# Performance work log

Hardware: AMD Instinct MI355X
Metric: run time of the kernel (lower is better)

Reference implementation:

```python
import jax, jax.numpy as jnp
import numpy as np

A = 15        # action_size
N = 3         # n_rollouts
TEMP = 1.0    # temperature
GAMMA = 0.99
D = 256       # state / embedder input dim
H = 256       # mid_weight == embedder output_dim
B = 32


def _mlp3(x, W0, b0, W1, b1, W2, b2):
    h = jax.nn.relu(x @ W0 + b0)
    h = jax.nn.relu(h @ W1 + b1)
    return h @ W2 + b2


def setup_inputs() -> dict:
    key = jax.random.key(0)
    ks = iter(jax.random.split(key, 32))

    def lin(i, o):
        return jax.random.normal(next(ks), (i, o), jnp.float32) * (1.0 / np.sqrt(i))

    inp = {"x": jax.random.normal(next(ks), (B, D), jnp.float32)}
    # embedder MLP: D -> H -> H -> H
    inp.update(emb_W0=lin(D, H), emb_b0=jnp.zeros((H,), jnp.float32),
               emb_W1=lin(H, H), emb_b1=jnp.zeros((H,), jnp.float32),
               emb_W2=lin(H, H), emb_b2=jnp.zeros((H,), jnp.float32))
    # fc_value: H -> 1
    inp.update(v_W=lin(H, 1), v_b=jnp.zeros((1,), jnp.float32))
    # cont_rew MLP: D+1 -> H -> H -> 2 (done logit, reward)
    inp.update(cr_W0=lin(D + 1, H), cr_b0=jnp.zeros((H,), jnp.float32),
               cr_W1=lin(H, H), cr_b1=jnp.zeros((H,), jnp.float32),
               cr_W2=lin(H, 2), cr_b2=jnp.zeros((2,), jnp.float32))
    # transition model MLP: D+1 -> H -> H -> D
    inp.update(tm_W0=lin(D + 1, H), tm_b0=jnp.zeros((H,), jnp.float32),
               tm_W1=lin(H, H), tm_b1=jnp.zeros((H,), jnp.float32),
               tm_W2=lin(H, D), tm_b2=jnp.zeros((D,), jnp.float32))
    return inp


def reference(x, emb_W0, emb_b0, emb_W1, emb_b1, emb_W2, emb_b2,
              v_W, v_b,
              cr_W0, cr_b0, cr_W1, cr_b1, cr_W2, cr_b2,
              tm_W0, tm_b0, tm_W1, tm_b1, tm_W2, tm_b2):
    def value(s):  # [..., D] -> [...]
        e = _mlp3(s, emb_W0, emb_b0, emb_W1, emb_b1, emb_W2, emb_b2)
        return (e @ v_W + v_b)[..., 0]

    acts = jnp.arange(A, dtype=x.dtype)

    v = value(x)  # [B]

    s = x
    rews, cont = [], []
    for _ in range(N):
        # states_with_all_actions: [..., A, D+1]
        sA = jnp.broadcast_to(s[..., None, :], s.shape[:-1] + (A, s.shape[-1]))
        aA = jnp.broadcast_to(acts, s.shape[:-1] + (A,))
        sa = jnp.concatenate([sA, aA[..., None]], axis=-1)
        dr = _mlp3(sa, cr_W0, cr_b0, cr_W1, cr_b1, cr_W2, cr_b2)  # [..., A, 2]
        cont.append(jax.nn.sigmoid(dr[..., 0]))
        rews.append(dr[..., 1])
        # transition for all actions at once; new action axis goes to dim 1
        ns = _mlp3(sa, tm_W0, tm_b0, tm_W1, tm_b1, tm_W2, tm_b2)  # [..., A, D]
        s = jnp.moveaxis(ns, -2, 1)

    cum = jnp.zeros_like(rews[0])  # [B, A]
    for r in rews[:-1]:
        c = (cum + r) * GAMMA
        cum = jnp.broadcast_to(c[..., None, :], c.shape[:-1] + (A,) + c.shape[-1:])

    vs = value(s) * (GAMMA ** N) + cum  # [B] + [A]*N
    for i in range(N - 1):
        vs = jnp.where(jnp.round(cont[-(i + 1)]) == 1, 0.0, vs)
        w = jax.nn.softmax(vs / TEMP, axis=-1)
        vs = (w * vs).sum(-1)

    log_probs = jax.nn.log_softmax(vs / TEMP, axis=1)  # [B, A]
    return log_probs, v
```

## Files before the change

kernel.cpp:

```cpp
#include <hip/hip_runtime.h>

#define NA 15
#define NB 32
#define DD 256
#define PL 65536
#define ASTR 264

using bf16x8 = __attribute__((ext_vector_type(8))) short;
using f32x4  = __attribute__((ext_vector_type(4))) float;

__device__ __forceinline__ unsigned short f2bf(float f){
  unsigned int u = __float_as_uint(f);
  u = u + 0x7fffu + ((u >> 16) & 1u);
  return (unsigned short)(u >> 16);
}
__device__ __forceinline__ float bf2f(unsigned short h){
  return __uint_as_float(((unsigned int)h) << 16);
}
__device__ __forceinline__ unsigned int cvtpk_bf16(float lo, float hi){
    unsigned int r;
    asm("v_cvt_pk_bf16_f32 %0, %1, %2" : "=v"(r) : "v"(lo), "v"(hi));
    return r;
}
__device__ __forceinline__ void split1_write(const float v[4], short* pH){
    unsigned int h01 = cvtpk_bf16(v[0], v[1]);
    unsigned int h23 = cvtpk_bf16(v[2], v[3]);
    *(uint2*)pH = make_uint2(h01, h23);
}
__device__ __forceinline__ void split2_write(const float v[4], short* pH, short* pL){
    unsigned int h01 = cvtpk_bf16(v[0], v[1]);
    unsigned int h23 = cvtpk_bf16(v[2], v[3]);
    float r0 = v[0] - __uint_as_float(h01 << 16);
    float r1 = v[1] - __uint_as_float(h01 & 0xffff0000u);
    float r2 = v[2] - __uint_as_float(h23 << 16);
    float r3 = v[3] - __uint_as_float(h23 & 0xffff0000u);
    unsigned int l01 = cvtpk_bf16(r0, r1);
    unsigned int l23 = cvtpk_bf16(r2, r3);
    *(uint2*)pH = make_uint2(h01, h23);
    *(uint2*)pL = make_uint2(l01, l23);
}
__device__ __forceinline__ void split3_write(const float v[4], short* pH, short* pM, short* pL){
    unsigned int h01 = cvtpk_bf16(v[0], v[1]);
    unsigned int h23 = cvtpk_bf16(v[2], v[3]);
    float r0 = v[0] - __uint_as_float(h01 << 16);
    float r1 = v[1] - __uint_as_float(h01 & 0xffff0000u);
    float r2 = v[2] - __uint_as_float(h23 << 16);
    float r3 = v[3] - __uint_as_float(h23 & 0xffff0000u);
    unsigned int m01 = cvtpk_bf16(r0, r1);
    unsigned int m23 = cvtpk_bf16(r2, r3);
    float s0 = r0 - __uint_as_float(m01 << 16);
    float s1 = r1 - __uint_as_float(m01 & 0xffff0000u);
    float s2 = r2 - __uint_as_float(m23 << 16);
    float s3 = r3 - __uint_as_float(m23 & 0xffff0000u);
    unsigned int l01 = cvtpk_bf16(s0, s1);
    unsigned int l23 = cvtpk_bf16(s2, s3);
    *(uint2*)pH = make_uint2(h01, h23);
    *(uint2*)pM = make_uint2(m01, m23);
    *(uint2*)pL = make_uint2(l01, l23);
}

template<int TM, bool RELU>
__device__ __forceinline__ void layer256(
    const float* __restrict__ W, const float* __restrict__ bias,
    const float* act, int K, int lda, float* out, int ldo)
{
    constexpr int RPG = TM / 4;
    const int tid = threadIdx.x;
    const int tr = tid >> 6;
    const int tc = tid & 63;
    float acc[RPG][4];
#pragma unroll
    for (int i = 0; i < RPG; ++i) { acc[i][0]=0.f; acc[i][1]=0.f; acc[i][2]=0.f; acc[i][3]=0.f; }
    const float* wp = W + 4 * tc;
    int k = 0;
    for (; k + 4 <= K; k += 4) {
        float4 w0 = *reinterpret_cast<const float4*>(wp + (k + 0) * DD);
        float4 w1 = *reinterpret_cast<const float4*>(wp + (k + 1) * DD);
        float4 w2 = *reinterpret_cast<const float4*>(wp + (k + 2) * DD);
        float4 w3 = *reinterpret_cast<const float4*>(wp + (k + 3) * DD);
#pragma unroll
        for (int i = 0; i < RPG; ++i) {
            float4 a = *reinterpret_cast<const float4*>(act + (RPG * tr + i) * lda + k);
            acc[i][0] += a.x * w0.x + a.y * w1.x + a.z * w2.x + a.w * w3.x;
            acc[i][1] += a.x * w0.y + a.y * w1.y + a.z * w2.y + a.w * w3.y;
            acc[i][2] += a.x * w0.z + a.y * w1.z + a.z * w2.z + a.w * w3.z;
            acc[i][3] += a.x * w0.w + a.y * w1.w + a.z * w2.w + a.w * w3.w;
        }
    }
    for (; k < K; ++k) {
        float4 w0 = *reinterpret_cast<const float4*>(wp + k * DD);
#pragma unroll
        for (int i = 0; i < RPG; ++i) {
            float a = act[(RPG * tr + i) * lda + k];
            acc[i][0] += a * w0.x; acc[i][1] += a * w0.y;
            acc[i][2] += a * w0.z; acc[i][3] += a * w0.w;
        }
    }
    float4 bb = *reinterpret_cast<const float4*>(bias + 4 * tc);
#pragma unroll
    for (int i = 0; i < RPG; ++i) {
        float4 o;
        o.x = acc[i][0] + bb.x; o.y = acc[i][1] + bb.y;
        o.z = acc[i][2] + bb.z; o.w = acc[i][3] + bb.w;
        if (RELU) {
            o.x = fmaxf(o.x, 0.f); o.y = fmaxf(o.y, 0.f);
            o.z = fmaxf(o.z, 0.f); o.w = fmaxf(o.w, 0.f);
        }
        *reinterpret_cast<float4*>(out + (RPG * tr + i) * ldo + 4 * tc) = o;
    }
}

template<int TM>
__device__ __forceinline__ void head1c(
    const float* h, int ldh, const float* __restrict__ W, int wstr, int col, float bias,
    float* __restrict__ gout, int gbase)
{
    const int wv = threadIdx.x >> 6;
    const int lane = threadIdx.x & 63;
    for (int rr = wv; rr < TM; rr += 4) {
        float p = 0.f;
#pragma unroll
        for (int t = 0; t < 4; ++t) {
            int k = lane + 64 * t;
            p += h[rr * ldh + k] * W[k * wstr + col];
        }
#pragma unroll
        for (int m = 1; m < 64; m <<= 1) p += __shfl_xor(p, m);
        if (lane == 0) gout[gbase + rr] = p + bias;
    }
}

__global__ __launch_bounds__(256) void front_kernel(
    const float* __restrict__ x,
    const float* __restrict__ emW0, const float* __restrict__ emB0,
    const float* __restrict__ emW1, const float* __restrict__ emB1,
    const float* __restrict__ emW2, const float* __restrict__ emB2,
    const float* __restrict__ vW, const float* __restrict__ vb,
    const float* __restrict__ crW0, const float* __restrict__ crW1,
    const float* __restrict__ tmW0, const float* __restrict__ tmW1,
    const float* __restrict__ tmW2, const float* __restrict__ tmB2,
    short* __restrict__ planes, float* __restrict__ w5, float* __restrict__ b5,
    float* __restrict__ c2cr, float* __restrict__ c2tm, float* __restrict__ b45,
    float* __restrict__ vout, float* __restrict__ U1cr, float* __restrict__ U1tm)
{
    __shared__ __align__(16) float smem[32 * DD];
    const int blk = blockIdx.x;
    const int tid = threadIdx.x;

    if (blk < 24) {
        const int mat = blk >> 3;
        const int kk  = blk & 7;
        const float* W = (mat == 0) ? crW1 : (mat == 1) ? tmW1 : emW1;
        const int col = tid;
        short bh[32], bm[32], bl[32];
#pragma unroll
        for (int j = 0; j < 32; ++j) {
            float w = W[(kk * 32 + j) * 256 + col];
            unsigned short h = f2bf(w); float fh = bf2f(h);
            float r1 = w - fh;
            unsigned short m = f2bf(r1); float fm = bf2f(m);
            bh[j] = (short)h; bm[j] = (short)m; bl[j] = (short)f2bf(r1 - fm);
        }
        short* pH = planes + (size_t)(mat * 3 + 0) * PL + kk * 8192 + col * 32;
        short* pM = planes + (size_t)(mat * 3 + 1) * PL + kk * 8192 + col * 32;
        short* pLp = planes + (size_t)(mat * 3 + 2) * PL + kk * 8192 + col * 32;
#pragma unroll
        for (int j = 0; j < 32; j += 4) {
            *(short4*)(pH + j) = make_short4(bh[j], bh[j+1], bh[j+2], bh[j+3]);
            *(short4*)(pM + j) = make_short4(bm[j], bm[j+1], bm[j+2], bm[j+3]);
            *(short4*)(pLp + j) = make_short4(bl[j], bl[j+1], bl[j+2], bl[j+3]);
        }
    } else if (blk == 24) {
        float acc = 0.f;
        for (int j = 0; j < 256; j += 4) {
            float4 wrow = *(const float4*)(emW2 + tid * 256 + j);
            float4 vv   = *(const float4*)(vW + j);
            acc += wrow.x * vv.x + wrow.y * vv.y + wrow.z * vv.z + wrow.w * vv.w;
        }
        w5[tid] = acc;
        if (tid == 0) {
            float b = 0.f;
            for (int j = 0; j < 256; ++j) b += emB2[j] * vW[j];
            b5[0] = b + vb[0];
        }
    } else if (blk < 33) {
        constexpr int TM = 4;
        float* bufA = smem;
        float* bufB = bufA + TM * DD;
        float* bufC = bufB + TM * DD;
        const int row0 = (blk - 25) * TM;
        for (int i = 0; i < TM; ++i) bufA[i * DD + tid] = x[(row0 + i) * DD + tid];
        __syncthreads();
        layer256<TM, true >(emW0, emB0, bufA, 256, DD, bufB, DD); __syncthreads();
        layer256<TM, true >(emW1, emB1, bufB, 256, DD, bufC, DD); __syncthreads();
        layer256<TM, false>(emW2, emB2, bufC, 256, DD, bufB, DD); __syncthreads();
        head1c<TM>(bufB, DD, vW, 1, 0, vb[0], vout, row0);
    } else if (blk < 41) {
        const int row0 = (blk - 33) * 4;
        float* xs = smem;
        for (int i = 0; i < 4; ++i) xs[i * 256 + tid] = x[(row0 + i) * 256 + tid];
        __syncthreads();
        float acr[4] = {0.f,0.f,0.f,0.f}, atm[4] = {0.f,0.f,0.f,0.f};
        for (int k = 0; k < 256; ++k) {
            float wc = crW0[k * 256 + tid];
            float wt = tmW0[k * 256 + tid];
#pragma unroll
            for (int i = 0; i < 4; ++i) {
                acr[i] += xs[i * 256 + k] * wc;
                atm[i] += xs[i * 256 + k] * wt;
            }
        }
        for (int i = 0; i < 4; ++i) {
            U1cr[(row0 + i) * 256 + tid] = acr[i];
            U1tm[(row0 + i) * 256 + tid] = atm[i];
        }
    } else if (blk < 65) {
        const int pb = blk - 41;
        const int prod = pb >> 3;
        const int r0 = (pb & 7) * 32;
        const float* B = (prod == 0) ? emW0 : (prod == 1) ? crW0 : tmW0;
        const int pbase = 9 + prod * 3;
        float* As = smem;
        for (int i = tid; i < 32 * 256; i += 256)
            As[i] = tmW2[(r0 + (i >> 8)) * 256 + (i & 255)];
        __syncthreads();
        float acc[32];
#pragma unroll
        for (int j = 0; j < 32; ++j) acc[j] = 0.f;
        for (int m = 0; m < 256; ++m) {
            float b = B[m * 256 + tid];
#pragma unroll
            for (int j = 0; j < 32; ++j) acc[j] += As[j * 256 + m] * b;
        }
        short bh[32], bm[32], bl[32];
#pragma unroll
        for (int j = 0; j < 32; ++j) {
            float w = acc[j];
            unsigned short h = f2bf(w); float fh = bf2f(h);
            float r1 = w - fh;
            unsigned short mm = f2bf(r1); float fm = bf2f(mm);
            bh[j] = (short)h; bm[j] = (short)mm; bl[j] = (short)f2bf(r1 - fm);
        }
        const int kk = r0 >> 5;
        short* pH = planes + (size_t)(pbase + 0) * PL + kk * 8192 + tid * 32;
        short* pM = planes + (size_t)(pbase + 1) * PL + kk * 8192 + tid * 32;
        short* pLp = planes + (size_t)(pbase + 2) * PL + kk * 8192 + tid * 32;
#pragma unroll
        for (int j = 0; j < 32; j += 4) {
            *(short4*)(pH + j) = make_short4(bh[j], bh[j+1], bh[j+2], bh[j+3]);
            *(short4*)(pM + j) = make_short4(bm[j], bm[j+1], bm[j+2], bm[j+3]);
            *(short4*)(pLp + j) = make_short4(bl[j], bl[j+1], bl[j+2], bl[j+3]);
        }
    } else {
        const int j = tid;
        float a0 = 0.f, a1 = 0.f, a2 = 0.f;
        for (int k = 0; k < 256; ++k) {
            float t = tmB2[k];
            a0 += t * crW0[k * 256 + j];
            a1 += t * tmW0[k * 256 + j];
            a2 += t * emW0[k * 256 + j];
        }
        c2cr[j] = a0;
        c2tm[j] = a1;
        b45[j] = a2 + emB0[j];
    }
}

__global__ __launch_bounds__(256) void finalize_kernel(
    const float* __restrict__ Vns3, const float* __restrict__ cont2,
    const float* __restrict__ rews0, const float* __restrict__ rews1,
    const float* __restrict__ cont1, float* __restrict__ out)
{
    const int b = blockIdx.x;
    const int tid = threadIdx.x;
    __shared__ float vs2[NA][NA];
    __shared__ float vs3[NA];
    if (tid < NA * NA) {
        const int x = tid / NA, y = tid % NA;
        float vals[NA];
        float m = -INFINITY;
#pragma unroll
        for (int z = 0; z < NA; ++z) {
            int vidx = ((b * NA + y) * NA + z) * NA + x;
            int cidx = ((b * NA + x) * NA + y) * NA + z;
            float c1 = rews0[b * NA + z] * 0.99f;
            float c2 = (c1 + rews1[(b * NA + x) * NA + z]) * 0.99f;
            float v = Vns3[vidx] * 0.970299f + c2;
            if (cont2[cidx] > 0.f) v = 0.f;
            vals[z] = v;
            m = fmaxf(m, v);
        }
        float se = 0.f, sw = 0.f;
#pragma unroll
        for (int z = 0; z < NA; ++z) { float e = expf(vals[z] - m); se += e; sw += e * vals[z]; }
        vs2[x][y] = sw / se;
    }
    __syncthreads();
    if (tid < NA) {
        const int x = tid;
        float vals[NA];
        float m = -INFINITY;
#pragma unroll
        for (int y = 0; y < NA; ++y) {
            float v = vs2[x][y];
            if (cont1[(b * NA + x) * NA + y] > 0.f) v = 0.f;
            vals[y] = v;
            m = fmaxf(m, v);
        }
        float se = 0.f, sw = 0.f;
#pragma unroll
        for (int y = 0; y < NA; ++y) { float e = expf(vals[y] - m); se += e; sw += e * vals[y]; }
        vs3[x] = sw / se;
    }
    __syncthreads();
    if (tid == 0) {
        float m = -INFINITY;
#pragma unroll
        for (int x = 0; x < NA; ++x) m = fmaxf(m, vs3[x]);
        float se = 0.f;
#pragma unroll
        for (int x = 0; x < NA; ++x) se += expf(vs3[x] - m);
        float l = logf(se);
#pragma unroll
        for (int x = 0; x < NA; ++x) out[b * NA + x] = vs3[x] - m - l;
    }
}

template<int RT, int NP>
__device__ __forceinline__ void mm3(
    const short* __restrict__ plH, const short* __restrict__ plM, const short* __restrict__ plL,
    const short* actH, const short* actM, const short* actL,
    f32x4 (&acc)[4][RT])
{
    const int tid = threadIdx.x;
    const int ln15 = tid & 15, lng = (tid >> 4) & 3, wv = tid >> 6;
    const int wo = (wv * 64 + ln15) * 32 + lng * 8;
#pragma unroll
    for (int kk = 0; kk < 8; ++kk) {
        bf16x8 wH[4], wM[4], wL[4], xH[RT], xM[RT], xL[RT];
#pragma unroll
        for (int ct = 0; ct < 4; ++ct) {
            wH[ct] = *(const bf16x8*)(plH + wo + kk * 8192 + ct * 512);
            wM[ct] = *(const bf16x8*)(plM + wo + kk * 8192 + ct * 512);
            if (NP == 6) wL[ct] = *(const bf16x8*)(plL + wo + kk * 8192 + ct * 512);
        }
#pragma unroll
        for (int rt = 0; rt < RT; ++rt) {
            int off = (rt * 16 + ln15) * ASTR + kk * 32 + lng * 8;
            xH[rt] = *(const bf16x8*)(actH + off);
            xM[rt] = *(const bf16x8*)(actM + off);
            if (NP == 6) xL[rt] = *(const bf16x8*)(actL + off);
        }
        __builtin_amdgcn_s_setprio(1);
#pragma unroll
        for (int ct = 0; ct < 4; ++ct)
#pragma unroll
            for (int rt = 0; rt < RT; ++rt) {
                acc[ct][rt] = __builtin_amdgcn_mfma_f32_16x16x32_bf16(wH[ct], xH[rt], acc[ct][rt], 0, 0, 0);
                acc[ct][rt] = __builtin_amdgcn_mfma_f32_16x16x32_bf16(wH[ct], xM[rt], acc[ct][rt], 0, 0, 0);
                acc[ct][rt] = __builtin_amdgcn_mfma_f32_16x16x32_bf16(wM[ct], xH[rt], acc[ct][rt], 0, 0, 0);
                if (NP == 6) {
                    acc[ct][rt] = __builtin_amdgcn_mfma_f32_16x16x32_bf16(wM[ct], xM[rt], acc[ct][rt], 0, 0, 0);
                    acc[ct][rt] = __builtin_amdgcn_mfma_f32_16x16x32_bf16(wH[ct], xL[rt], acc[ct][rt], 0, 0, 0);
                    acc[ct][rt] = __builtin_amdgcn_mfma_f32_16x16x32_bf16(wL[ct], xH[rt], acc[ct][rt], 0, 0, 0);
                }
            }
        __builtin_amdgcn_s_setprio(0);
    }
}

template<int ROWS, bool CLAMP>
__device__ __forceinline__ void stage3w(
    const float* __restrict__ U, const float* __restrict__ wrow256,
    const float* __restrict__ bias, int row0,
    short* actH, short* actM, short* actL)
{
    const int tid = threadIdx.x;
    const int wv = tid >> 6, ln = tid & 63;
    constexpr int RPW = ROWS / 4;
    const float4 wr = *(const float4*)(wrow256 + ln * 4);
    const float4 bb = *(const float4*)(bias + ln * 4);
    for (int i = wv * RPW; i < wv * RPW + RPW; ++i) {
        int r = row0 + i;
        int srow = r / 15;
        if (CLAMP && srow > 7199) srow = 7199;
        float a = (float)(r % 15);
        float4 u = *(const float4*)(U + srow * 256 + ln * 4);
        float sv[4];
        sv[0] = fmaxf(u.x + a * wr.x + bb.x, 0.f);
        sv[1] = fmaxf(u.y + a * wr.y + bb.y, 0.f);
        sv[2] = fmaxf(u.z + a * wr.z + bb.z, 0.f);
        sv[3] = fmaxf(u.w + a * wr.w + bb.w, 0.f);
        split3_write(sv, actH + i * ASTR + ln * 4, actM + i * ASTR + ln * 4, actL + i * ASTR + ln * 4);
    }
}

__global__ __launch_bounds__(256, 2) void stage1m_kernel(
    const float* __restrict__ U1cr, const float* __restrict__ U1tm,
    const short* __restrict__ planes,
    const float* __restrict__ crW0, const float* __restrict__ crB0,
    const float* __restrict__ crB1, const float* __restrict__ crW2, const float* __restrict__ crB2,
    const float* __restrict__ tmW0, const float* __restrict__ tmB0,
    const float* __restrict__ tmB1,
    const float* __restrict__ c2cr, const float* __restrict__ c2tm,
    float* __restrict__ rews0, float* __restrict__ U2cr, float* __restrict__ U2tm)
{
    __shared__ short actH[16 * ASTR];
    __shared__ short actM[16 * ASTR];
    __shared__ short actL[16 * ASTR];
    __shared__ float hred[64];
    const int tid = threadIdx.x;
    const int row0 = blockIdx.x * 16;
    const int ln15 = tid & 15, lng = (tid >> 4) & 3, wv = tid >> 6;

    stage3w<16, false>(U1cr, crW0 + 65536, crB0, row0, actH, actM, actL);
    __syncthreads();
    {
        f32x4 acc[4][1];
#pragma unroll
        for (int a = 0; a < 4; ++a) acc[a][0] = f32x4{0.f,0.f,0.f,0.f};
        mm3<1, 6>(planes + 0*PL, planes + 1*PL, planes + 2*PL, actH, actM, actL, acc);
        float hp = 0.f;
#pragma unroll
        for (int ct = 0; ct < 4; ++ct) {
            const int colb = wv * 64 + ct * 16 + lng * 4;
            const float4 b1 = *(const float4*)(crB1 + colb);
            f32x4 v = acc[ct][0];
            v[0] += b1.x; v[1] += b1.y; v[2] += b1.z; v[3] += b1.w;
#pragma unroll
            for (int j = 0; j < 4; ++j) v[j] = fmaxf(v[j], 0.f);
#pragma unroll
            for (int j = 0; j < 4; ++j) hp += v[j] * crW2[(colb + j) * 2 + 1];
        }
        hp += __shfl_xor(hp, 16);
        hp += __shfl_xor(hp, 32);
        if (lng == 0) hred[wv * 16 + ln15] = hp;
        __syncthreads();
        if (tid < 16) rews0[row0 + tid] = hred[tid] + hred[16 + tid] + hred[32 + tid] + hred[48 + tid] + crB2[1];
        __syncthreads();
    }

    stage3w<16, false>(U1tm, tmW0 + 65536, tmB0, row0, actH, actM, actL);
    __syncthreads();
    {
        f32x4 acc[4][1];
#pragma unroll
        for (int a = 0; a < 4; ++a) acc[a][0] = f32x4{0.f,0.f,0.f,0.f};
        mm3<1, 6>(planes + 3*PL, planes + 4*PL, planes + 5*PL, actH, actM, actL, acc);
        __syncthreads();
#pragma unroll
        for (int ct = 0; ct < 4; ++ct) {
            const int colb = wv * 64 + ct * 16 + lng * 4;
            const float4 bb = *(const float4*)(tmB1 + colb);
            f32x4 v = acc[ct][0];
            v[0] += bb.x; v[1] += bb.y; v[2] += bb.z; v[3] += bb.w;
#pragma unroll
            for (int j = 0; j < 4; ++j) v[j] = fmaxf(v[j], 0.f);
            float sv[4] = {v[0], v[1], v[2], v[3]};
            const int ao = ln15 * ASTR + colb;
            split3_write(sv, actH + ao, actM + ao, actL + ao);
        }
        __syncthreads();
    }
    {
        f32x4 acc[4][1];
#pragma unroll
        for (int a = 0; a < 4; ++a) acc[a][0] = f32x4{0.f,0.f,0.f,0.f};
        mm3<1, 6>(planes + 12*PL, planes + 13*PL, planes + 14*PL, actH, actM, actL, acc);
#pragma unroll
        for (int ct = 0; ct < 4; ++ct) {
            const int colb = wv * 64 + ct * 16 + lng * 4;
            const float4 cc = *(const float4*)(c2cr + colb);
            float4 o; o.x = acc[ct][0][0] + cc.x; o.y = acc[ct][0][1] + cc.y;
            o.z = acc[ct][0][2] + cc.z; o.w = acc[ct][0][3] + cc.w;
            *(float4*)(U2cr + (row0 + ln15) * 256 + colb) = o;
        }
    }
    {
        f32x4 acc[4][1];
#pragma unroll
        for (int a = 0; a < 4; ++a) acc[a][0] = f32x4{0.f,0.f,0.f,0.f};
        mm3<1, 6>(planes + 15*PL, planes + 16*PL, planes + 17*PL, actH, actM, actL, acc);
#pragma unroll
        for (int ct = 0; ct < 4; ++ct) {
            const int colb = wv * 64 + ct * 16 + lng * 4;
            const float4 cc = *(const float4*)(c2tm + colb);
            float4 o; o.x = acc[ct][0][0] + cc.x; o.y = acc[ct][0][1] + cc.y;
            o.z = acc[ct][0][2] + cc.z; o.w = acc[ct][0][3] + cc.w;
            *(float4*)(U2tm + (row0 + ln15) * 256 + colb) = o;
        }
    }
}

__global__ __launch_bounds__(256, 2) void stage2m_kernel(
    const float* __restrict__ U2cr, const float* __restrict__ U2tm,
    const short* __restrict__ planes,
    const float* __restrict__ crW0, const float* __restrict__ crB0,
    const float* __restrict__ crB1, const float* __restrict__ crW2, const float* __restrict__ crB2,
    const float* __restrict__ tmW0, const float* __restrict__ tmB0,
    const float* __restrict__ tmB1,
    const float* __restrict__ c2cr, const float* __restrict__ c2tm,
    float* __restrict__ cont1, float* __restrict__ rews1,
    float* __restrict__ Ucr, float* __restrict__ Utm)
{
    __shared__ short actH[16 * ASTR];
    __shared__ short actM[16 * ASTR];
    __shared__ short actL[16 * ASTR];
    __shared__ float hred[2][64];
    const int tid = threadIdx.x;
    const int row0 = blockIdx.x * 16;
    const int ln15 = tid & 15, lng = (tid >> 4) & 3, wv = tid >> 6;

    stage3w<16, false>(U2cr, crW0 + 65536, crB0, row0, actH, actM, actL);
    __syncthreads();
    {
        f32x4 acc[4][1];
#pragma unroll
        for (int a = 0; a < 4; ++a) acc[a][0] = f32x4{0.f,0.f,0.f,0.f};
        mm3<1, 6>(planes + 0*PL, planes + 1*PL, planes + 2*PL, actH, actM, actL, acc);
        float hp0 = 0.f, hp1 = 0.f;
#pragma unroll
        for (int ct = 0; ct < 4; ++ct) {
            const int colb = wv * 64 + ct * 16 + lng * 4;
            const float4 b1 = *(const float4*)(crB1 + colb);
            f32x4 v = acc[ct][0];
            v[0] += b1.x; v[1] += b1.y; v[2] += b1.z; v[3] += b1.w;
#pragma unroll
            for (int j = 0; j < 4; ++j) v[j] = fmaxf(v[j], 0.f);
#pragma unroll
            for (int j = 0; j < 4; ++j) {
                hp0 += v[j] * crW2[(colb + j) * 2 + 0];
                hp1 += v[j] * crW2[(colb + j) * 2 + 1];
            }
        }
        hp0 += __shfl_xor(hp0, 16); hp0 += __shfl_xor(hp0, 32);
        hp1 += __shfl_xor(hp1, 16); hp1 += __shfl_xor(hp1, 32);
        if (lng == 0) {
            hred[0][wv * 16 + ln15] = hp0;
            hred[1][wv * 16 + ln15] = hp1;
        }
        __syncthreads();
        if (tid < 16)
            cont1[row0 + tid] = hred[0][tid] + hred[0][16 + tid] + hred[0][32 + tid] + hred[0][48 + tid] + crB2[0];
        else if (tid >= 64 && tid < 80)
            rews1[row0 + tid - 64] = hred[1][tid - 64] + hred[1][16 + tid - 64] + hred[1][32 + tid - 64] + hred[1][48 + tid - 64] + crB2[1];
        __syncthreads();
    }

    stage3w<16, false>(U2tm, tmW0 + 65536, tmB0, row0, actH, actM, actL);
    __syncthreads();
    {
        f32x4 acc[4][1];
#pragma unroll
        for (int a = 0; a < 4; ++a) acc[a][0] = f32x4{0.f,0.f,0.f,0.f};
        mm3<1, 6>(planes + 3*PL, planes + 4*PL, planes + 5*PL, actH, actM, actL, acc);
        __syncthreads();
#pragma unroll
        for (int ct = 0; ct < 4; ++ct) {
            const int colb = wv * 64 + ct * 16 + lng * 4;
            const float4 bb = *(const float4*)(tmB1 + colb);
            f32x4 v = acc[ct][0];
            v[0] += bb.x; v[1] += bb.y; v[2] += bb.z; v[3] += bb.w;
#pragma unroll
            for (int j = 0; j < 4; ++j) v[j] = fmaxf(v[j], 0.f);
            float sv[4] = {v[0], v[1], v[2], v[3]};
            const int ao = ln15 * ASTR + colb;
            split3_write(sv, actH + ao, actM + ao, actL + ao);
        }
        __syncthreads();
    }
    int pr;
    {
        int r = row0 + ln15;
        int b = r / 225, a1 = (r / 15) % 15, a2 = r % 15;
        pr = (b * 15 + a2) * 15 + a1;
    }
    {
        f32x4 acc[4][1];
#pragma unroll
        for (int a = 0; a < 4; ++a) acc[a][0] = f32x4{0.f,0.f,0.f,0.f};
        mm3<1, 6>(planes + 12*PL, planes + 13*PL, planes + 14*PL, actH, actM, actL, acc);
#pragma unroll
        for (int ct = 0; ct < 4; ++ct) {
            const int colb = wv * 64 + ct * 16 + lng * 4;
            const float4 cc = *(const float4*)(c2cr + colb);
            float4 o; o.x = acc[ct][0][0] + cc.x; o.y = acc[ct][0][1] + cc.y;
            o.z = acc[ct][0][2] + cc.z; o.w = acc[ct][0][3] + cc.w;
            *(float4*)(Ucr + pr * 256 + colb) = o;
        }
    }
    {
        f32x4 acc[4][1];
#pragma unroll
        for (int a = 0; a < 4; ++a) acc[a][0] = f32x4{0.f,0.f,0.f,0.f};
        mm3<1, 3>(planes + 15*PL, planes + 16*PL, planes + 17*PL, actH, actM, actL, acc);
#pragma unroll
        for (int ct = 0; ct < 4; ++ct) {
            const int colb = wv * 64 + ct * 16 + lng * 4;
            const float4 cc = *(const float4*)(c2tm + colb);
            float4 o; o.x = acc[ct][0][0] + cc.x; o.y = acc[ct][0][1] + cc.y;
            o.z = acc[ct][0][2] + cc.z; o.w = acc[ct][0][3] + cc.w;
            *(float4*)(Utm + pr * 256 + colb) = o;
        }
    }
}

template<int RT, bool RELU, bool HEAD, bool WRITEACT>
__device__ __forceinline__ void layer_b1(
    const short* __restrict__ plH,
    const float* __restrict__ bias,
    const float* __restrict__ headW, const float* __restrict__ headB,
    float* __restrict__ headOut, int row0,
    short* actH, float* hred)
{
    const int tid = threadIdx.x;
    const int ln15 = tid & 15, lng = (tid >> 4) & 3, wv = tid >> 6;
    const int wo = (wv * 64 + ln15) * 32 + lng * 8;
    f32x4 acc[4][RT];
#pragma unroll
    for (int a = 0; a < 4; ++a)
#pragma unroll
        for (int b = 0; b < RT; ++b) acc[a][b] = f32x4{0.f, 0.f, 0.f, 0.f};

#pragma unroll
    for (int kk = 0; kk < 8; ++kk) {
        bf16x8 aH[4], bH[RT];
#pragma unroll
        for (int ct = 0; ct < 4; ++ct)
            aH[ct] = *(const bf16x8*)(plH + wo + kk * 8192 + ct * 512);
#pragma unroll
        for (int rt = 0; rt < RT; ++rt) {
            int off = (rt * 16 + ln15) * ASTR + kk * 32 + lng * 8;
            bH[rt] = *(const bf16x8*)(actH + off);
        }
        __builtin_amdgcn_s_setprio(1);
#pragma unroll
        for (int ct = 0; ct < 4; ++ct)
#pragma unroll
            for (int rt = 0; rt < RT; ++rt)
                acc[ct][rt] = __builtin_amdgcn_mfma_f32_16x16x32_bf16(aH[ct], bH[rt], acc[ct][rt], 0, 0, 0);
        __builtin_amdgcn_s_setprio(0);
    }
    __syncthreads();

    float hp[RT];
#pragma unroll
    for (int rt = 0; rt < RT; ++rt) hp[rt] = 0.f;
#pragma unroll
    for (int ct = 0; ct < 4; ++ct) {
        const int colb = wv * 64 + ct * 16 + lng * 4;
        const float4 bb = *(const float4*)(bias + colb);
#pragma unroll
        for (int rt = 0; rt < RT; ++rt) {
            f32x4 v = acc[ct][rt];
            v[0] += bb.x; v[1] += bb.y; v[2] += bb.z; v[3] += bb.w;
            if (RELU) {
#pragma unroll
                for (int j = 0; j < 4; ++j) v[j] = fmaxf(v[j], 0.f);
            }
            if (HEAD) {
                const float4 hw = *(const float4*)(headW + colb);
                hp[rt] += v[0] * hw.x + v[1] * hw.y + v[2] * hw.z + v[3] * hw.w;
            }
            if (WRITEACT) {
                float sv[4] = {v[0], v[1], v[2], v[3]};
                const int ao = (rt * 16 + ln15) * ASTR + colb;
                split1_write(sv, actH + ao);
            }
        }
    }
    if constexpr (HEAD) {
        constexpr int NR = RT * 16;
#pragma unroll
        for (int rt = 0; rt < RT; ++rt) {
            hp[rt] += __shfl_xor(hp[rt], 16);
            hp[rt] += __shfl_xor(hp[rt], 32);
        }
        if (lng == 0) {
#pragma unroll
            for (int rt = 0; rt < RT; ++rt) hred[wv * NR + rt * 16 + ln15] = hp[rt];
        }
        __syncthreads();
        if (tid < NR && row0 + tid < 108000) {
            float s = hred[tid] + hred[NR + tid] + hred[2 * NR + tid] + hred[3 * NR + tid] + headB[0];
            headOut[row0 + tid] = s;
        }
    }
    if constexpr (WRITEACT) __syncthreads();
}

__global__ __launch_bounds__(256, 2) void k3ab_kernel(
    const float* __restrict__ Ucr, const float* __restrict__ Utm,
    const short* __restrict__ planes,
    const float* __restrict__ crW0, const float* __restrict__ crB0,
    const float* __restrict__ crB1, const float* __restrict__ crW2,
    const float* __restrict__ crB2,
    const float* __restrict__ tmW0, const float* __restrict__ tmB0,
    const float* __restrict__ tmB1,
    const float* __restrict__ b45, const float* __restrict__ emB1,
    const float* __restrict__ w5, const float* __restrict__ b5,
    float* __restrict__ cont2, float* __restrict__ Vns3)
{
    __shared__ short lds[3 * 48 * ASTR];
    __shared__ float hred[512];
    const int tid = threadIdx.x;
    const int g = blockIdx.x / 11, rm = blockIdx.x % 11;
    bool isB; int idx;
    if (g < 281) {
        isB = rm < 3;
        idx = isB ? (g * 3 + rm) : (g * 8 + (rm - 3));
    } else {
        isB = rm < 1;
        idx = isB ? 843 : (2248 + (rm - 1));
    }
    const int ln15 = tid & 15, lng = (tid >> 4) & 3, wv = tid >> 6;
    const short* P = planes;

    if (isB) {
        const int row0 = idx * 128;
        short* actH = lds;
        const int ln = tid & 63;
        const float4 wr = *(const float4*)(tmW0 + 65536 + ln * 4);
        const float4 bb = *(const float4*)(tmB0 + ln * 4);
        for (int i = wv * 32; i < wv * 32 + 32; ++i) {
            int r = row0 + i;
            int srow = r / 15;
            if (srow > 7199) srow = 7199;
            float a = (float)(r % 15);
            float4 u = *(const float4*)(Utm + srow * 256 + ln * 4);
            float sv[4];
            sv[0] = fmaxf(u.x + a * wr.x + bb.x, 0.f);
            sv[1] = fmaxf(u.y + a * wr.y + bb.y, 0.f);
            sv[2] = fmaxf(u.z + a * wr.z + bb.z, 0.f);
            sv[3] = fmaxf(u.w + a * wr.w + bb.w, 0.f);
            split1_write(sv, actH + i * ASTR + ln * 4);
        }
        __syncthreads();
        layer_b1<8, true,  false, true >(P + 3 * PL, tmB1, nullptr, nullptr, nullptr, row0, actH, hred);
        layer_b1<8, true,  false, true >(P + 9 * PL, b45,  nullptr, nullptr, nullptr, row0, actH, hred);
        layer_b1<8, true,  true,  false>(P + 6 * PL, emB1, w5, b5, Vns3, row0, actH, hred);
    } else {
        const int row0 = idx * 48;
        short* actH = lds;
        short* actM = lds + 48 * ASTR;
        short* actL = lds + 2 * 48 * ASTR;
        stage3w<48, false>(Ucr, crW0 + 65536, crB0, row0, actH, actM, actL);
        __syncthreads();
        f32x4 acc[4][3];
#pragma unroll
        for (int a = 0; a < 4; ++a)
#pragma unroll
            for (int b = 0; b < 3; ++b) acc[a][b] = f32x4{0.f,0.f,0.f,0.f};
        mm3<3, 6>(P + 0*PL, P + 1*PL, P + 2*PL, actH, actM, actL, acc);
        float hp[3] = {0.f, 0.f, 0.f};
#pragma unroll
        for (int ct = 0; ct < 4; ++ct) {
            const int colb = wv * 64 + ct * 16 + lng * 4;
            const float4 b1 = *(const float4*)(crB1 + colb);
#pragma unroll
            for (int rt = 0; rt < 3; ++rt) {
                f32x4 v = acc[ct][rt];
                v[0] += b1.x; v[1] += b1.y; v[2] += b1.z; v[3] += b1.w;
#pragma unroll
                for (int j = 0; j < 4; ++j) v[j] = fmaxf(v[j], 0.f);
#pragma unroll
                for (int j = 0; j < 4; ++j) hp[rt] += v[j] * crW2[(colb + j) * 2];
            }
        }
#pragma unroll
        for (int rt = 0; rt < 3; ++rt) {
            hp[rt] += __shfl_xor(hp[rt], 16);
            hp[rt] += __shfl_xor(hp[rt], 32);
        }
        if (lng == 0) {
#pragma unroll
            for (int rt = 0; rt < 3; ++rt) hred[wv * 48 + rt * 16 + ln15] = hp[rt];
        }
        __syncthreads();
        if (tid < 48)
            cont2[row0 + tid] = hred[tid] + hred[48 + tid] + hred[96 + tid] + hred[144 + tid] + crB2[0];
    }
}

extern "C" void kernel_launch(void* const* d_in, const int* in_sizes, int n_in,
                              void* d_out, int out_size, void* d_ws, size_t ws_size,
                              hipStream_t stream)
{
    (void)in_sizes; (void)n_in; (void)out_size; (void)ws_size;
    const float* x    = (const float*)d_in[0];
    const float* emW0 = (const float*)d_in[1];
    const float* emB0 = (const float*)d_in[2];
    const float* emW1 = (const float*)d_in[3];
    const float* emB1 = (const float*)d_in[4];
    const float* emW2 = (const float*)d_in[5];
    const float* emB2 = (const float*)d_in[6];
    const float* vW   = (const float*)d_in[7];
    const float* vb   = (const float*)d_in[8];
    const float* crW0 = (const float*)d_in[9];
    const float* crB0 = (const float*)d_in[10];
    const float* crW1 = (const float*)d_in[11];
    const float* crB1 = (const float*)d_in[12];
    const float* crW2 = (const float*)d_in[13];
    const float* crB2 = (const float*)d_in[14];
    const float* tmW0 = (const float*)d_in[15];
    const float* tmB0 = (const float*)d_in[16];
    const float* tmW1 = (const float*)d_in[17];
    const float* tmB1 = (const float*)d_in[18];
    const float* tmW2 = (const float*)d_in[19];
    const float* tmB2 = (const float*)d_in[20];
    float* out = (float*)d_out;

    float* w     = (float*)d_ws;
    float* rews0 = w;
    float* cont1 = rews0 + 480;
    float* rews1 = cont1 + 7200;
    float* cont2 = rews1 + 7200;
    float* Vns3  = cont2 + 108000;
    float* U1cr  = Vns3 + 108000;
    float* U1tm  = U1cr + 32 * 256;
    short* planes = (short*)(U1tm + 32 * 256);
    float* U2cr  = (float*)(planes + 18 * PL);
    float* U2tm  = U2cr + 480 * 256;
    float* Ucr   = U2tm + 480 * 256;
    float* Utm   = Ucr + 7200 * 256;
    float* w5    = Utm + 7200 * 256;
    float* b5    = w5 + 256;
    float* c2cr  = b5 + 4;
    float* c2tm  = c2cr + 256;
    float* b45   = c2tm + 256;

    front_kernel<<<66, 256, 0, stream>>>(x,
        emW0, emB0, emW1, emB1, emW2, emB2, vW, vb,
        crW0, crW1, tmW0, tmW1, tmW2, tmB2,
        planes, w5, b5, c2cr, c2tm, b45,
        out + NB * NA, U1cr, U1tm);
    stage1m_kernel<<<30, 256, 0, stream>>>(U1cr, U1tm, planes,
        crW0, crB0, crB1, crW2, crB2, tmW0, tmB0, tmB1,
        c2cr, c2tm, rews0, U2cr, U2tm);
    stage2m_kernel<<<450, 256, 0, stream>>>(U2cr, U2tm, planes,
        crW0, crB0, crB1, crW2, crB2, tmW0, tmB0, tmB1,
        c2cr, c2tm, cont1, rews1, Ucr, Utm);
    k3ab_kernel<<<3094, 256, 0, stream>>>(Ucr, Utm, planes,
        crW0, crB0, crB1, crW2, crB2,
        tmW0, tmB0, tmB1, b45, emB1, w5, b5, cont2, Vns3);
    finalize_kernel<<<NB, 256, 0, stream>>>(Vns3, cont2, rews0, rews1, cont1, out);
}
```

Measured before the change: 244.3 us.

## Use two-plane bf16 split for cont/reward MLP and retile k3ab blocks

```diff
diff --git a/kernel.cpp b/kernel.cpp
--- a/kernel.cpp
+++ b/kernel.cpp
@@ -369,6 +369,43 @@
     }
 }
 
+template<int RT>
+__device__ __forceinline__ void mm24(
+    const short* __restrict__ plH, const short* __restrict__ plM,
+    const short* actH, const short* actL,
+    f32x4 (&acc)[4][RT])
+{
+    const int tid = threadIdx.x;
+    const int ln15 = tid & 15, lng = (tid >> 4) & 3, wv = tid >> 6;
+    const int wo = (wv * 64 + ln15) * 32 + lng * 8;
+#pragma unroll
+    for (int kk = 0; kk < 8; ++kk) {
+        bf16x8 wH[4], wM[4], xH[RT], xL[RT];
+#pragma unroll
+        for (int ct = 0; ct < 4; ++ct) {
+            wH[ct] = *(const bf16x8*)(plH + wo + kk * 8192 + ct * 512);
+            wM[ct] = *(const bf16x8*)(plM + wo + kk * 8192 + ct * 512);
+        }
+#pragma unroll
+        for (int rt = 0; rt < RT; ++rt) {
+            int off = (rt * 16 + ln15) * ASTR + kk * 32 + lng * 8;
+            xH[rt] = *(const bf16x8*)(actH + off);
+            xL[rt] = *(const bf16x8*)(actL + off);
+        }
+        __builtin_amdgcn_s_setprio(1);
+#pragma unroll
+        for (int ct = 0; ct < 4; ++ct)
+#pragma unroll
+            for (int rt = 0; rt < RT; ++rt) {
+                acc[ct][rt] = __builtin_amdgcn_mfma_f32_16x16x32_bf16(wH[ct], xH[rt], acc[ct][rt], 0, 0, 0);
+                acc[ct][rt] = __builtin_amdgcn_mfma_f32_16x16x32_bf16(wH[ct], xL[rt], acc[ct][rt], 0, 0, 0);
+                acc[ct][rt] = __builtin_amdgcn_mfma_f32_16x16x32_bf16(wM[ct], xH[rt], acc[ct][rt], 0, 0, 0);
+                acc[ct][rt] = __builtin_amdgcn_mfma_f32_16x16x32_bf16(wM[ct], xL[rt], acc[ct][rt], 0, 0, 0);
+            }
+        __builtin_amdgcn_s_setprio(0);
+    }
+}
+
 template<int ROWS, bool CLAMP>
 __device__ __forceinline__ void stage3w(
     const float* __restrict__ U, const float* __restrict__ wrow256,
@@ -395,6 +432,32 @@
     }
 }
 
+template<int ROWS, bool CLAMP>
+__device__ __forceinline__ void stage2wact(
+    const float* __restrict__ U, const float* __restrict__ wrow256,
+    const float* __restrict__ bias, int row0,
+    short* actH, short* actL)
+{
+    const int tid = threadIdx.x;
+    const int wv = tid >> 6, ln = tid & 63;
+    constexpr int RPW = ROWS / 4;
+    const float4 wr = *(const float4*)(wrow256 + ln * 4);
+    const float4 bb = *(const float4*)(bias + ln * 4);
+    for (int i = wv * RPW; i < wv * RPW + RPW; ++i) {
+        int r = row0 + i;
+        int srow = r / 15;
+        if (CLAMP && srow > 7199) srow = 7199;
+        float a = (float)(r % 15);
+        float4 u = *(const float4*)(U + srow * 256 + ln * 4);
+        float sv[4];
+        sv[0] = fmaxf(u.x + a * wr.x + bb.x, 0.f);
+        sv[1] = fmaxf(u.y + a * wr.y + bb.y, 0.f);
+        sv[2] = fmaxf(u.z + a * wr.z + bb.z, 0.f);
+        sv[3] = fmaxf(u.w + a * wr.w + bb.w, 0.f);
+        split2_write(sv, actH + i * ASTR + ln * 4, actL + i * ASTR + ln * 4);
+    }
+}
+
 __global__ __launch_bounds__(256, 2) void stage1m_kernel(
     const float* __restrict__ U1cr, const float* __restrict__ U1tm,
     const short* __restrict__ planes,
@@ -413,13 +476,13 @@
     const int row0 = blockIdx.x * 16;
     const int ln15 = tid & 15, lng = (tid >> 4) & 3, wv = tid >> 6;
 
-    stage3w<16, false>(U1cr, crW0 + 65536, crB0, row0, actH, actM, actL);
+    stage2wact<16, false>(U1cr, crW0 + 65536, crB0, row0, actH, actL);
     __syncthreads();
     {
         f32x4 acc[4][1];
 #pragma unroll
         for (int a = 0; a < 4; ++a) acc[a][0] = f32x4{0.f,0.f,0.f,0.f};
-        mm3<1, 6>(planes + 0*PL, planes + 1*PL, planes + 2*PL, actH, actM, actL, acc);
+        mm24<1>(planes + 0*PL, planes + 1*PL, actH, actL, acc);
         float hp = 0.f;
 #pragma unroll
         for (int ct = 0; ct < 4; ++ct) {
@@ -511,13 +574,13 @@
     const int row0 = blockIdx.x * 16;
     const int ln15 = tid & 15, lng = (tid >> 4) & 3, wv = tid >> 6;
 
-    stage3w<16, false>(U2cr, crW0 + 65536, crB0, row0, actH, actM, actL);
+    stage2wact<16, false>(U2cr, crW0 + 65536, crB0, row0, actH, actL);
     __syncthreads();
     {
         f32x4 acc[4][1];
 #pragma unroll
         for (int a = 0; a < 4; ++a) acc[a][0] = f32x4{0.f,0.f,0.f,0.f};
-        mm3<1, 6>(planes + 0*PL, planes + 1*PL, planes + 2*PL, actH, actM, actL, acc);
+        mm24<1>(planes + 0*PL, planes + 1*PL, actH, actL, acc);
         float hp0 = 0.f, hp1 = 0.f;
 #pragma unroll
         for (int ct = 0; ct < 4; ++ct) {
@@ -701,28 +764,22 @@
     const float* __restrict__ w5, const float* __restrict__ b5,
     float* __restrict__ cont2, float* __restrict__ Vns3)
 {
-    __shared__ short lds[3 * 48 * ASTR];
-    __shared__ float hred[512];
-    const int tid = threadIdx.x;
-    const int g = blockIdx.x / 11, rm = blockIdx.x % 11;
-    bool isB; int idx;
-    if (g < 281) {
-        isB = rm < 3;
-        idx = isB ? (g * 3 + rm) : (g * 8 + (rm - 3));
-    } else {
-        isB = rm < 1;
-        idx = isB ? 843 : (2248 + (rm - 1));
-    }
+    __shared__ short lds[144 * ASTR];
+    __shared__ float hred[576];
+    const int tid = threadIdx.x;
+    const int g = blockIdx.x / 10, rm = blockIdx.x % 10;
+    const bool isB = rm < 3;
+    const int idx = isB ? (g * 3 + rm) : (g * 7 + (rm - 3));
     const int ln15 = tid & 15, lng = (tid >> 4) & 3, wv = tid >> 6;
     const short* P = planes;
 
     if (isB) {
-        const int row0 = idx * 128;
+        const int row0 = idx * 144;
         short* actH = lds;
         const int ln = tid & 63;
         const float4 wr = *(const float4*)(tmW0 + 65536 + ln * 4);
         const float4 bb = *(const float4*)(tmB0 + ln * 4);
-        for (int i = wv * 32; i < wv * 32 + 32; ++i) {
+        for (int i = wv * 36; i < wv * 36 + 36; ++i) {
             int r = row0 + i;
             int srow = r / 15;
             if (srow > 7199) srow = 7199;
@@ -736,29 +793,29 @@
             split1_write(sv, actH + i * ASTR + ln * 4);
         }
         __syncthreads();
-        layer_b1<8, true,  false, true >(P + 3 * PL, tmB1, nullptr, nullptr, nullptr, row0, actH, hred);
-        layer_b1<8, true,  false, true >(P + 9 * PL, b45,  nullptr, nullptr, nullptr, row0, actH, hred);
-        layer_b1<8, true,  true,  false>(P + 6 * PL, emB1, w5, b5, Vns3, row0, actH, hred);
+        layer_b1<9, true,  false, true >(P + 3 * PL, tmB1, nullptr, nullptr, nullptr, row0, actH, hred);
+        layer_b1<9, true,  false, true >(P + 9 * PL, b45,  nullptr, nullptr, nullptr, row0, actH, hred);
+        layer_b1<9, true,  true,  false>(P + 6 * PL, emB1, w5, b5, Vns3, row0, actH, hred);
     } else {
-        const int row0 = idx * 48;
+        if (idx >= 1688) return;
+        const int row0 = idx * 64;
         short* actH = lds;
-        short* actM = lds + 48 * ASTR;
-        short* actL = lds + 2 * 48 * ASTR;
-        stage3w<48, false>(Ucr, crW0 + 65536, crB0, row0, actH, actM, actL);
-        __syncthreads();
-        f32x4 acc[4][3];
+        short* actL = lds + 64 * ASTR;
+        stage2wact<64, true>(Ucr, crW0 + 65536, crB0, row0, actH, actL);
+        __syncthreads();
+        f32x4 acc[4][4];
 #pragma unroll
         for (int a = 0; a < 4; ++a)
 #pragma unroll
-            for (int b = 0; b < 3; ++b) acc[a][b] = f32x4{0.f,0.f,0.f,0.f};
-        mm3<3, 6>(P + 0*PL, P + 1*PL, P + 2*PL, actH, actM, actL, acc);
-        float hp[3] = {0.f, 0.f, 0.f};
+            for (int b = 0; b < 4; ++b) acc[a][b] = f32x4{0.f,0.f,0.f,0.f};
+        mm24<4>(P + 0*PL, P + 1*PL, actH, actL, acc);
+        float hp[4] = {0.f, 0.f, 0.f, 0.f};
 #pragma unroll
         for (int ct = 0; ct < 4; ++ct) {
             const int colb = wv * 64 + ct * 16 + lng * 4;
             const float4 b1 = *(const float4*)(crB1 + colb);
 #pragma unroll
-            for (int rt = 0; rt < 3; ++rt) {
+            for (int rt = 0; rt < 4; ++rt) {
                 f32x4 v = acc[ct][rt];
                 v[0] += b1.x; v[1] += b1.y; v[2] += b1.z; v[3] += b1.w;
 #pragma unroll
@@ -768,17 +825,17 @@
             }
         }
 #pragma unroll
-        for (int rt = 0; rt < 3; ++rt) {
+        for (int rt = 0; rt < 4; ++rt) {
             hp[rt] += __shfl_xor(hp[rt], 16);
             hp[rt] += __shfl_xor(hp[rt], 32);
         }
         if (lng == 0) {
 #pragma unroll
-            for (int rt = 0; rt < 3; ++rt) hred[wv * 48 + rt * 16 + ln15] = hp[rt];
-        }
-        __syncthreads();
-        if (tid < 48)
-            cont2[row0 + tid] = hred[tid] + hred[48 + tid] + hred[96 + tid] + hred[144 + tid] + crB2[0];
+            for (int rt = 0; rt < 4; ++rt) hred[wv * 64 + rt * 16 + ln15] = hp[rt];
+        }
+        __syncthreads();
+        if (tid < 64 && row0 + tid < 108000)
+            cont2[row0 + tid] = hred[tid] + hred[64 + tid] + hred[128 + tid] + hred[192 + tid] + crB2[0];
     }
 }
 
@@ -840,7 +897,7 @@
     stage2m_kernel<<<450, 256, 0, stream>>>(U2cr, U2tm, planes,
         crW0, crB0, crB1, crW2, crB2, tmW0, tmB0, tmB1,
         c2cr, c2tm, cont1, rews1, Ucr, Utm);
-    k3ab_kernel<<<3094, 256, 0, stream>>>(Ucr, Utm, planes,
+    k3ab_kernel<<<2500, 256, 0, stream>>>(Ucr, Utm, planes,
         crW0, crB0, crB1, crW2, crB2,
         tmW0, tmB0, tmB1, b45, emB1, w5, b5, cont2, Vns3);
     finalize_kernel<<<NB, 256, 0, stream>>>(Vns3, cont2, rews0, rews1, cont1, out);
```

After: 221.2 us. 9.4% less time.
